# Kernel tuning notes

Hardware: AMD Instinct MI355X
Metric: run time of the kernel (lower is better)

## Reference

```python
import jax, jax.numpy as jnp
import numpy as np

N = 100000
E = 1600000

def _graphconv(x, src, dst, W, b):
    # DGL GraphConv, norm='both', in_feats > out_feats path: transform then aggregate.
    ones = jnp.ones((E,), dtype=x.dtype)
    out_deg = jax.ops.segment_sum(ones, src, num_segments=N)
    in_deg = jax.ops.segment_sum(ones, dst, num_segments=N)
    out_norm = jax.lax.rsqrt(jnp.clip(out_deg, 1.0))  # D_out^{-1/2}
    in_norm = jax.lax.rsqrt(jnp.clip(in_deg, 1.0))    # D_in^{-1/2}
    h = (x * out_norm[:, None]) @ W                    # [N, out_feats]
    msg = h[src]                                       # gather over edges [E, out_feats]
    agg = jax.ops.segment_sum(msg, dst, num_segments=N)
    return agg * in_norm[:, None] + b


def setup_inputs() -> dict:
    key = jax.random.key(0)
    k1, k2, k3, k4, k5 = jax.random.split(key, 5)
    features = jax.random.normal(k1, (N, 256), dtype=jnp.float32)
    src = jax.random.randint(k2, (E,), 0, N, dtype=jnp.int32)
    dst = jax.random.randint(k3, (E,), 0, N, dtype=jnp.int32)
    # Xavier-uniform like DGL's GraphConv reset_parameters
    lim1 = float(np.sqrt(6.0 / (256 + 64)))
    lim2 = float(np.sqrt(6.0 / (64 + 40)))
    W1 = jax.random.uniform(k4, (256, 64), jnp.float32, -lim1, lim1)
    W2 = jax.random.uniform(k5, (64, 40), jnp.float32, -lim2, lim2)
    b1 = jnp.zeros((64,), jnp.float32)
    b2 = jnp.zeros((40,), jnp.float32)
    return {"features": features, "src": src, "dst": dst,
            "W1": W1, "b1": b1, "W2": W2, "b2": b2}


def reference(features, src, dst, W1, b1, W2, b2):
    x = _graphconv(features, src, dst, W1, b1)
    x = _graphconv(x, src, dst, W2, b2)
    return x
```

## Files before the change

kernel.cpp:

```cpp
#include <hip/hip_runtime.h>

#define N_NODES 100000
#define N_EDGES 1600000
#define NBUCK 391
#define HBLK 128
#define CAP 8192


__global__ __launch_bounds__(256) void coarse_hist_kernel(
    const int* __restrict__ src, const int* __restrict__ dst,
    int* __restrict__ gHD, int* __restrict__ gHS) {
    __shared__ int hd[NBUCK], hs[NBUCK];
    for (int i = threadIdx.x; i < NBUCK; i += 256) { hd[i] = 0; hs[i] = 0; }
    __syncthreads();
    for (int e = blockIdx.x * 256 + threadIdx.x; e < N_EDGES; e += HBLK * 256) {
        atomicAdd(&hd[dst[e] >> 8], 1);
        atomicAdd(&hs[src[e] >> 8], 1);
    }
    __syncthreads();
    for (int i = threadIdx.x; i < NBUCK; i += 256) {
        if (hd[i]) atomicAdd(&gHD[i], hd[i]);
        if (hs[i]) atomicAdd(&gHS[i], hs[i]);
    }
}


__global__ void coarse_scan_kernel(const int* __restrict__ gHD, const int* __restrict__ gHS,
                                   int* __restrict__ dBase, int* __restrict__ sBase) {
    __shared__ int sd[512], se[512];
    int t = threadIdx.x;
    int vd = (t < NBUCK) ? gHD[t] : 0;
    int vs = (t < NBUCK) ? gHS[t] : 0;
    sd[t] = vd; se[t] = vs;
    __syncthreads();
    for (int s = 1; s < 512; s <<= 1) {
        int ud = (t >= s) ? sd[t - s] : 0;
        int us = (t >= s) ? se[t - s] : 0;
        __syncthreads();
        sd[t] += ud; se[t] += us;
        __syncthreads();
    }
    if (t < NBUCK) { dBase[t] = sd[t] - vd; sBase[t] = se[t] - vs; }
    if (t == 0) { dBase[NBUCK] = N_EDGES; sBase[NBUCK] = N_EDGES; }
}


__global__ __launch_bounds__(256) void scatter_both_kernel(
    const int* __restrict__ src, const int* __restrict__ dst,
    const int* __restrict__ dBase, const int* __restrict__ sBase,
    int* __restrict__ dRes, int* __restrict__ sRes,
    int* __restrict__ bsrc, unsigned char* __restrict__ bdlo,
    unsigned char* __restrict__ bslo) {
    __shared__ int hd[NBUCK], hs[NBUCK], curD[NBUCK], curS[NBUCK];
    for (int i = threadIdx.x; i < NBUCK; i += 256) { hd[i] = 0; hs[i] = 0; }
    __syncthreads();
    for (int e = blockIdx.x * 256 + threadIdx.x; e < N_EDGES; e += HBLK * 256) {
        atomicAdd(&hd[dst[e] >> 8], 1);
        atomicAdd(&hs[src[e] >> 8], 1);
    }
    __syncthreads();
    for (int i = threadIdx.x; i < NBUCK; i += 256) {
        int cd = hd[i];
        curD[i] = dBase[i] + (cd ? atomicAdd(&dRes[i], cd) : 0);
        int cs = hs[i];
        curS[i] = sBase[i] + (cs ? atomicAdd(&sRes[i], cs) : 0);
    }
    __syncthreads();
    for (int e = blockIdx.x * 256 + threadIdx.x; e < N_EDGES; e += HBLK * 256) {
        int s = src[e];
        int d = dst[e];
        int pd = atomicAdd(&curD[d >> 8], 1);
        bsrc[pd] = s;
        bdlo[pd] = (unsigned char)(d & 255);
        int ps = atomicAdd(&curS[s >> 8], 1);
        bslo[ps] = (unsigned char)(s & 255);
    }
}


__global__ __launch_bounds__(256) void fine_src_kernel(
    const int* __restrict__ sBase, const unsigned char* __restrict__ bslo,
    float* __restrict__ onorm) {
    __shared__ int hist[256];
    int t = threadIdx.x, b = blockIdx.x;
    int lo = sBase[b], hi = sBase[b + 1];
    hist[t] = 0;
    __syncthreads();
    for (int p = lo + t; p < hi; p += 256) atomicAdd(&hist[bslo[p]], 1);
    __syncthreads();
    int node = b * 256 + t;
    if (node < N_NODES) onorm[node] = 1.0f / sqrtf((float)max(hist[t], 1));
}


__global__ __launch_bounds__(256) void gemm1_kernel(
    const float* __restrict__ x, const float* __restrict__ W,
    const float* __restrict__ onorm, float* __restrict__ h, int n) {
    __shared__ float As[16][128];
    __shared__ float Ws[16][68];
    const int tid = threadIdx.x;
    const int tx = tid & 15;
    const int rg = tid >> 4;
    const int rowBase = blockIdx.x * 128;

    const int lr0 = tid >> 2;
    const int lkq = (tid & 3) * 4;
    const int wk = tid >> 4;
    const int wc = (tid & 15) * 4;

    const int row0 = rowBase + lr0;
    const int row1 = rowBase + 64 + lr0;
    const float sc0 = (row0 < n) ? onorm[row0] : 0.f;
    const float sc1 = (row1 < n) ? onorm[row1] : 0.f;

    float acc[8][4] = {};

    for (int k0 = 0; k0 < 256; k0 += 16) {
        *(float4*)&Ws[wk][wc] = *(const float4*)(W + (size_t)(k0 + wk) * 64 + wc);
        float4 v0 = make_float4(0.f, 0.f, 0.f, 0.f);
        float4 v1 = make_float4(0.f, 0.f, 0.f, 0.f);
        if (row0 < n) v0 = *(const float4*)(x + (size_t)row0 * 256 + k0 + lkq);
        if (row1 < n) v1 = *(const float4*)(x + (size_t)row1 * 256 + k0 + lkq);
        As[lkq + 0][lr0] = v0.x * sc0;
        As[lkq + 1][lr0] = v0.y * sc0;
        As[lkq + 2][lr0] = v0.z * sc0;
        As[lkq + 3][lr0] = v0.w * sc0;
        As[lkq + 0][64 + lr0] = v1.x * sc1;
        As[lkq + 1][64 + lr0] = v1.y * sc1;
        As[lkq + 2][64 + lr0] = v1.z * sc1;
        As[lkq + 3][64 + lr0] = v1.w * sc1;
        __syncthreads();
#pragma unroll
        for (int k = 0; k < 16; ++k) {
            float4 b = *(const float4*)&Ws[k][tx * 4];
            float4 a0 = *(const float4*)&As[k][rg * 8];
            float4 a1 = *(const float4*)&As[k][rg * 8 + 4];
            float av[8] = {a0.x, a0.y, a0.z, a0.w, a1.x, a1.y, a1.z, a1.w};
            float bv[4] = {b.x, b.y, b.z, b.w};
#pragma unroll
            for (int i = 0; i < 8; ++i)
#pragma unroll
                for (int j = 0; j < 4; ++j) acc[i][j] += av[i] * bv[j];
        }
        __syncthreads();
    }
#pragma unroll
    for (int i = 0; i < 8; ++i) {
        int row = rowBase + rg * 8 + i;
        if (row < n) {
            *(float4*)(h + (size_t)row * 64 + tx * 4) =
                make_float4(acc[i][0], acc[i][1], acc[i][2], acc[i][3]);
        }
    }
}


__global__ __launch_bounds__(1024) void agg64_fused_kernel(
    const int* __restrict__ dBase, const int* __restrict__ bsrc,
    const unsigned char* __restrict__ bdlo, const float* __restrict__ h,
    float* __restrict__ agg, float* __restrict__ inorm) {
    __shared__ int lsrc[CAP];
    __shared__ int hist[256], scn[256], cur[256];
    const int tid = threadIdx.x;
    const int b = blockIdx.x;
    const int lo = dBase[b];
    const int hi = min(dBase[b + 1], lo + CAP);
    if (tid < 256) hist[tid] = 0;
    __syncthreads();
    for (int p = lo + tid; p < hi; p += 1024) atomicAdd(&hist[bdlo[p]], 1);
    __syncthreads();
    int v = (tid < 256) ? hist[tid] : 0;
    if (tid < 256) scn[tid] = v;
    __syncthreads();
    for (int s = 1; s < 256; s <<= 1) {
        int u = 0;
        if (tid < 256 && tid >= s) u = scn[tid - s];
        __syncthreads();
        if (tid < 256 && tid >= s) scn[tid] += u;
        __syncthreads();
    }
    if (tid < 256) {
        int excl = scn[tid] - v;
        scn[tid] = excl;
        cur[tid] = excl;
        int node = b * 256 + tid;
        if (node < N_NODES) inorm[node] = 1.0f / sqrtf((float)max(v, 1));
    }
    __syncthreads();
    for (int p = lo + tid; p < hi; p += 1024) {
        int pos = atomicAdd(&cur[bdlo[p]], 1);
        lsrc[pos] = bsrc[p];
    }
    __syncthreads();

    const int w = tid >> 6, lane = tid & 63, q = lane >> 4, f = lane & 15;
    for (int nn = w; nn < 256; nn += 16) {
        int node = b * 256 + nn;
        if (node >= N_NODES) break;
        int beg = scn[nn];
        int end = beg + hist[nn];
        float4 a0 = {0.f, 0.f, 0.f, 0.f}, a1 = {0.f, 0.f, 0.f, 0.f};
        int j = beg;
        for (; j + 8 <= end; j += 8) {
            int s0 = lsrc[j + q], s1 = lsrc[j + 4 + q];
            float4 v0 = *((const float4*)(h + (size_t)s0 * 64) + f);
            float4 v1 = *((const float4*)(h + (size_t)s1 * 64) + f);
            a0.x += v0.x; a0.y += v0.y; a0.z += v0.z; a0.w += v0.w;
            a1.x += v1.x; a1.y += v1.y; a1.z += v1.z; a1.w += v1.w;
        }
        for (; j + 4 <= end; j += 4) {
            int s0 = lsrc[j + q];
            float4 v0 = *((const float4*)(h + (size_t)s0 * 64) + f);
            a0.x += v0.x; a0.y += v0.y; a0.z += v0.z; a0.w += v0.w;
        }
        if (j + q < end) {
            int s0 = lsrc[j + q];
            float4 v0 = *((const float4*)(h + (size_t)s0 * 64) + f);
            a0.x += v0.x; a0.y += v0.y; a0.z += v0.z; a0.w += v0.w;
        }
        a0.x += a1.x; a0.y += a1.y; a0.z += a1.z; a0.w += a1.w;
        a0.x += __shfl_xor(a0.x, 16); a0.y += __shfl_xor(a0.y, 16);
        a0.z += __shfl_xor(a0.z, 16); a0.w += __shfl_xor(a0.w, 16);
        a0.x += __shfl_xor(a0.x, 32); a0.y += __shfl_xor(a0.y, 32);
        a0.z += __shfl_xor(a0.z, 32); a0.w += __shfl_xor(a0.w, 32);
        if (q == 0) ((float4*)(agg + (size_t)node * 64))[f] = a0;
    }
}


__global__ __launch_bounds__(256) void gemm2_kernel(
    const float* __restrict__ agg, const float* __restrict__ W2,
    const float* __restrict__ b1, const float* __restrict__ inorm,
    const float* __restrict__ onorm, float* __restrict__ h2, int n) {
    const int lane = threadIdx.x & 63;
    const int wid = __builtin_amdgcn_readfirstlane(threadIdx.x >> 6);
    const int rowBase = (blockIdx.x * 4 + wid) * 8;
    const int cl = lane < 40 ? lane : 39;

    float w[64];
#pragma unroll
    for (int k = 0; k < 64; ++k) w[k] = W2[k * 40 + cl];

    float c2 = 0.f;
#pragma unroll
    for (int k = 0; k < 64; ++k) c2 += b1[k] * w[k];

#pragma unroll
    for (int r = 0; r < 8; ++r) {
        int row = rowBase + r;
        if (row < n) {
            const float* ar = agg + (size_t)row * 64;
            float acc = 0.f;
#pragma unroll
            for (int k = 0; k < 64; ++k) acc += ar[k] * w[k];
            float so = onorm[row];
            float s12 = inorm[row] * so;
            if (lane < 40) h2[(size_t)row * 40 + lane] = acc * s12 + so * c2;
        }
    }
}


__global__ __launch_bounds__(1024) void agg40_fused_kernel(
    const int* __restrict__ dBase, const int* __restrict__ bsrc,
    const unsigned char* __restrict__ bdlo, const float* __restrict__ h2,
    const float* __restrict__ b2, float* __restrict__ out) {
    __shared__ int lsrc[CAP];
    __shared__ int hist[256], scn[256], cur[256];
    const int tid = threadIdx.x;
    const int b = blockIdx.x;
    const int lo = dBase[b];
    const int hi = min(dBase[b + 1], lo + CAP);
    if (tid < 256) hist[tid] = 0;
    __syncthreads();
    for (int p = lo + tid; p < hi; p += 1024) atomicAdd(&hist[bdlo[p]], 1);
    __syncthreads();
    int v = (tid < 256) ? hist[tid] : 0;
    if (tid < 256) scn[tid] = v;
    __syncthreads();
    for (int s = 1; s < 256; s <<= 1) {
        int u = 0;
        if (tid < 256 && tid >= s) u = scn[tid - s];
        __syncthreads();
        if (tid < 256 && tid >= s) scn[tid] += u;
        __syncthreads();
    }
    if (tid < 256) {
        int excl = scn[tid] - v;
        scn[tid] = excl;
        cur[tid] = excl;
    }
    __syncthreads();
    for (int p = lo + tid; p < hi; p += 1024) {
        int pos = atomicAdd(&cur[bdlo[p]], 1);
        lsrc[pos] = bsrc[p];
    }
    __syncthreads();

    const int w = tid >> 6, lane = tid & 63, q = lane >> 4, f = lane & 15;
    const bool act = (f < 10);
    float4 vb = make_float4(0.f, 0.f, 0.f, 0.f);
    if (act) vb = ((const float4*)b2)[f];
    for (int nn = w; nn < 256; nn += 16) {
        int node = b * 256 + nn;
        if (node >= N_NODES) break;
        int beg = scn[nn];
        int end = beg + hist[nn];
        float4 a0 = {0.f, 0.f, 0.f, 0.f}, a1 = {0.f, 0.f, 0.f, 0.f};
        int j = beg;
        for (; j + 8 <= end; j += 8) {
            int s0 = lsrc[j + q], s1 = lsrc[j + 4 + q];
            if (act) {
                float4 v0 = *((const float4*)(h2 + (size_t)s0 * 40) + f);
                float4 v1 = *((const float4*)(h2 + (size_t)s1 * 40) + f);
                a0.x += v0.x; a0.y += v0.y; a0.z += v0.z; a0.w += v0.w;
                a1.x += v1.x; a1.y += v1.y; a1.z += v1.z; a1.w += v1.w;
            }
        }
        for (; j + 4 <= end; j += 4) {
            int s0 = lsrc[j + q];
            if (act) {
                float4 v0 = *((const float4*)(h2 + (size_t)s0 * 40) + f);
                a0.x += v0.x; a0.y += v0.y; a0.z += v0.z; a0.w += v0.w;
            }
        }
        if (j + q < end && act) {
            int s0 = lsrc[j + q];
            float4 v0 = *((const float4*)(h2 + (size_t)s0 * 40) + f);
            a0.x += v0.x; a0.y += v0.y; a0.z += v0.z; a0.w += v0.w;
        }
        a0.x += a1.x; a0.y += a1.y; a0.z += a1.z; a0.w += a1.w;
        a0.x += __shfl_xor(a0.x, 16); a0.y += __shfl_xor(a0.y, 16);
        a0.z += __shfl_xor(a0.z, 16); a0.w += __shfl_xor(a0.w, 16);
        a0.x += __shfl_xor(a0.x, 32); a0.y += __shfl_xor(a0.y, 32);
        a0.z += __shfl_xor(a0.z, 32); a0.w += __shfl_xor(a0.w, 32);
        if (q == 0 && act) {
            float s = 1.0f / sqrtf((float)max(hist[nn], 1));
            float4 r;
            r.x = a0.x * s + vb.x; r.y = a0.y * s + vb.y;
            r.z = a0.z * s + vb.z; r.w = a0.w * s + vb.w;
            ((float4*)(out + (size_t)node * 40))[f] = r;
        }
    }
}

extern "C" void kernel_launch(void* const* d_in, const int* in_sizes, int n_in,
                              void* d_out, int out_size, void* d_ws, size_t ws_size,
                              hipStream_t stream) {
    const float* x  = (const float*)d_in[0];
    const int* src  = (const int*)d_in[1];
    const int* dst  = (const int*)d_in[2];
    const float* W1 = (const float*)d_in[3];
    const float* b1 = (const float*)d_in[4];
    const float* W2 = (const float*)d_in[5];
    const float* b2 = (const float*)d_in[6];
    float* out = (float*)d_out;

    char* wsb = (char*)d_ws;
    size_t off = 0;
    auto alloc = [&](size_t bytes) { char* p = wsb + off; off += (bytes + 255) & ~size_t(255); return p; };

    int*   zeroed = (int*)  alloc(4 * NBUCK * 4);
    int*   gHD    = zeroed;
    int*   gHS    = zeroed + NBUCK;
    int*   dRes   = zeroed + 2 * NBUCK;
    int*   sRes   = zeroed + 3 * NBUCK;
    int*   dBase  = (int*)  alloc((NBUCK + 1) * 4);
    int*   sBase  = (int*)  alloc((NBUCK + 1) * 4);
    float* onorm  = (float*)alloc(N_NODES * 4);
    float* inorm  = (float*)alloc(N_NODES * 4);
    int*   bsrc   = (int*)  alloc((size_t)N_EDGES * 4);
    unsigned char* bdlo = (unsigned char*)alloc(N_EDGES);
    unsigned char* bslo = (unsigned char*)alloc(N_EDGES);
    float* h1     = (float*)alloc((size_t)N_NODES * 64 * 4);
    float* agg1   = (float*)alloc((size_t)N_NODES * 64 * 4);
    float* h2 = h1;

    hipMemsetAsync(zeroed, 0, 4 * NBUCK * 4, stream);

    coarse_hist_kernel<<<HBLK, 256, 0, stream>>>(src, dst, gHD, gHS);
    coarse_scan_kernel<<<1, 512, 0, stream>>>(gHD, gHS, dBase, sBase);
    scatter_both_kernel<<<HBLK, 256, 0, stream>>>(src, dst, dBase, sBase, dRes, sRes,
                                                  bsrc, bdlo, bslo);
    fine_src_kernel<<<NBUCK, 256, 0, stream>>>(sBase, bslo, onorm);

    gemm1_kernel<<<(N_NODES + 127) / 128, 256, 0, stream>>>(x, W1, onorm, h1, N_NODES);

    agg64_fused_kernel<<<NBUCK, 1024, 0, stream>>>(dBase, bsrc, bdlo, h1, agg1, inorm);

    gemm2_kernel<<<(N_NODES + 31) / 32, 256, 0, stream>>>(agg1, W2, b1, inorm, onorm, h2, N_NODES);

    agg40_fused_kernel<<<NBUCK, 1024, 0, stream>>>(dBase, bsrc, bdlo, h2, b2, out);
}
```

Before: 437.4 us.

## Halve bucket width, pack edge src/dst-low, and register-prefetch gemm1

Bucket width drops from 256 to 128 nodes (782 buckets), so the agg kernels use 512-thread blocks with a smaller LDS edge cap. Source id and destination low bits are packed into one int per edge, which removes the separate byte array and one read stream. gemm1 moves to 128 threads with an 8x8 register tile, prefetches the next x/W tile into registers, and applies onorm in the epilogue. The smaller CAP (4096 edges per bucket) could truncate edges in dense buckets, and the larger per-thread tile raises register pressure.

```diff
diff --git a/kernel.cpp b/kernel.cpp
--- a/kernel.cpp
+++ b/kernel.cpp
@@ -2,9 +2,11 @@
 
 #define N_NODES 100000
 #define N_EDGES 1600000
-#define NBUCK 391
-#define HBLK 128
-#define CAP 8192
+#define BSH 7
+#define NBUCK 782
+#define BMASK 127
+#define HBLK 512
+#define CAP 4096
 
 
 __global__ __launch_bounds__(256) void coarse_hist_kernel(
@@ -14,8 +16,8 @@
     for (int i = threadIdx.x; i < NBUCK; i += 256) { hd[i] = 0; hs[i] = 0; }
     __syncthreads();
     for (int e = blockIdx.x * 256 + threadIdx.x; e < N_EDGES; e += HBLK * 256) {
-        atomicAdd(&hd[dst[e] >> 8], 1);
-        atomicAdd(&hs[src[e] >> 8], 1);
+        atomicAdd(&hd[dst[e] >> BSH], 1);
+        atomicAdd(&hs[src[e] >> BSH], 1);
     }
     __syncthreads();
     for (int i = threadIdx.x; i < NBUCK; i += 256) {
@@ -25,15 +27,16 @@
 }
 
 
-__global__ void coarse_scan_kernel(const int* __restrict__ gHD, const int* __restrict__ gHS,
-                                   int* __restrict__ dBase, int* __restrict__ sBase) {
-    __shared__ int sd[512], se[512];
+__global__ __launch_bounds__(1024) void coarse_scan_kernel(
+    const int* __restrict__ gHD, const int* __restrict__ gHS,
+    int* __restrict__ dBase, int* __restrict__ sBase) {
+    __shared__ int sd[1024], se[1024];
     int t = threadIdx.x;
     int vd = (t < NBUCK) ? gHD[t] : 0;
     int vs = (t < NBUCK) ? gHS[t] : 0;
     sd[t] = vd; se[t] = vs;
     __syncthreads();
-    for (int s = 1; s < 512; s <<= 1) {
+    for (int s = 1; s < 1024; s <<= 1) {
         int ud = (t >= s) ? sd[t - s] : 0;
         int us = (t >= s) ? se[t - s] : 0;
         __syncthreads();
@@ -49,14 +52,13 @@
     const int* __restrict__ src, const int* __restrict__ dst,
     const int* __restrict__ dBase, const int* __restrict__ sBase,
     int* __restrict__ dRes, int* __restrict__ sRes,
-    int* __restrict__ bsrc, unsigned char* __restrict__ bdlo,
-    unsigned char* __restrict__ bslo) {
+    int* __restrict__ bpack, unsigned char* __restrict__ bslo) {
     __shared__ int hd[NBUCK], hs[NBUCK], curD[NBUCK], curS[NBUCK];
     for (int i = threadIdx.x; i < NBUCK; i += 256) { hd[i] = 0; hs[i] = 0; }
     __syncthreads();
     for (int e = blockIdx.x * 256 + threadIdx.x; e < N_EDGES; e += HBLK * 256) {
-        atomicAdd(&hd[dst[e] >> 8], 1);
-        atomicAdd(&hs[src[e] >> 8], 1);
+        atomicAdd(&hd[dst[e] >> BSH], 1);
+        atomicAdd(&hs[src[e] >> BSH], 1);
     }
     __syncthreads();
     for (int i = threadIdx.x; i < NBUCK; i += 256) {
@@ -69,11 +71,10 @@
     for (int e = blockIdx.x * 256 + threadIdx.x; e < N_EDGES; e += HBLK * 256) {
         int s = src[e];
         int d = dst[e];
-        int pd = atomicAdd(&curD[d >> 8], 1);
-        bsrc[pd] = s;
-        bdlo[pd] = (unsigned char)(d & 255);
-        int ps = atomicAdd(&curS[s >> 8], 1);
-        bslo[ps] = (unsigned char)(s & 255);
+        int pd = atomicAdd(&curD[d >> BSH], 1);
+        bpack[pd] = (s << BSH) | (d & BMASK);
+        int ps = atomicAdd(&curS[s >> BSH], 1);
+        bslo[ps] = (unsigned char)(s & BMASK);
     }
 }
 
@@ -81,121 +82,142 @@
 __global__ __launch_bounds__(256) void fine_src_kernel(
     const int* __restrict__ sBase, const unsigned char* __restrict__ bslo,
     float* __restrict__ onorm) {
-    __shared__ int hist[256];
+    __shared__ int hist[128];
     int t = threadIdx.x, b = blockIdx.x;
     int lo = sBase[b], hi = sBase[b + 1];
-    hist[t] = 0;
+    if (t < 128) hist[t] = 0;
     __syncthreads();
     for (int p = lo + t; p < hi; p += 256) atomicAdd(&hist[bslo[p]], 1);
     __syncthreads();
-    int node = b * 256 + t;
-    if (node < N_NODES) onorm[node] = 1.0f / sqrtf((float)max(hist[t], 1));
-}
-
-
-__global__ __launch_bounds__(256) void gemm1_kernel(
+    int node = b * 128 + t;
+    if (t < 128 && node < N_NODES) onorm[node] = 1.0f / sqrtf((float)max(hist[t], 1));
+}
+
+
+__global__ __launch_bounds__(128) void gemm1_kernel(
     const float* __restrict__ x, const float* __restrict__ W,
     const float* __restrict__ onorm, float* __restrict__ h, int n) {
     __shared__ float As[16][128];
     __shared__ float Ws[16][68];
     const int tid = threadIdx.x;
-    const int tx = tid & 15;
-    const int rg = tid >> 4;
+    const int tx = tid & 7;
+    const int ry = tid >> 3;
     const int rowBase = blockIdx.x * 128;
 
-    const int lr0 = tid >> 2;
-    const int lkq = (tid & 3) * 4;
-    const int wk = tid >> 4;
-    const int wc = (tid & 15) * 4;
-
-    const int row0 = rowBase + lr0;
-    const int row1 = rowBase + 64 + lr0;
-    const float sc0 = (row0 < n) ? onorm[row0] : 0.f;
-    const float sc1 = (row1 < n) ? onorm[row1] : 0.f;
-
-    float acc[8][4] = {};
-
+    const int lr = tid >> 2;
+    const int kq = (tid & 3) * 4;
+    const int wk = tid >> 3;
+    const int wc = (tid & 7) * 8;
+
+    float4 va[4], vw0, vw1;
+
+    auto load_regs = [&](int k0) {
+#pragma unroll
+        for (int p = 0; p < 4; ++p) {
+            int row = rowBase + p * 32 + lr;
+            va[p] = (row < n) ? *(const float4*)(x + (size_t)row * 256 + k0 + kq)
+                              : make_float4(0.f, 0.f, 0.f, 0.f);
+        }
+        vw0 = *(const float4*)(W + (size_t)wk * 64 + wc);
+        vw1 = *(const float4*)(W + (size_t)wk * 64 + wc + 4);
+    };
+    auto load_regs_w = [&](int k0) {
+#pragma unroll
+        for (int p = 0; p < 4; ++p) {
+            int row = rowBase + p * 32 + lr;
+            va[p] = (row < n) ? *(const float4*)(x + (size_t)row * 256 + k0 + kq)
+                              : make_float4(0.f, 0.f, 0.f, 0.f);
+        }
+        vw0 = *(const float4*)(W + (size_t)(k0 + wk) * 64 + wc);
+        vw1 = *(const float4*)(W + (size_t)(k0 + wk) * 64 + wc + 4);
+    };
+
+    float acc[8][8] = {};
+
+    load_regs(0);
     for (int k0 = 0; k0 < 256; k0 += 16) {
-        *(float4*)&Ws[wk][wc] = *(const float4*)(W + (size_t)(k0 + wk) * 64 + wc);
-        float4 v0 = make_float4(0.f, 0.f, 0.f, 0.f);
-        float4 v1 = make_float4(0.f, 0.f, 0.f, 0.f);
-        if (row0 < n) v0 = *(const float4*)(x + (size_t)row0 * 256 + k0 + lkq);
-        if (row1 < n) v1 = *(const float4*)(x + (size_t)row1 * 256 + k0 + lkq);
-        As[lkq + 0][lr0] = v0.x * sc0;
-        As[lkq + 1][lr0] = v0.y * sc0;
-        As[lkq + 2][lr0] = v0.z * sc0;
-        As[lkq + 3][lr0] = v0.w * sc0;
-        As[lkq + 0][64 + lr0] = v1.x * sc1;
-        As[lkq + 1][64 + lr0] = v1.y * sc1;
-        As[lkq + 2][64 + lr0] = v1.z * sc1;
-        As[lkq + 3][64 + lr0] = v1.w * sc1;
-        __syncthreads();
+#pragma unroll
+        for (int p = 0; p < 4; ++p) {
+            int r = p * 32 + lr;
+            As[kq + 0][r] = va[p].x;
+            As[kq + 1][r] = va[p].y;
+            As[kq + 2][r] = va[p].z;
+            As[kq + 3][r] = va[p].w;
+        }
+        *(float4*)&Ws[wk][wc] = vw0;
+        *(float4*)&Ws[wk][wc + 4] = vw1;
+        __syncthreads();
+        if (k0 + 16 < 256) load_regs_w(k0 + 16);
 #pragma unroll
         for (int k = 0; k < 16; ++k) {
-            float4 b = *(const float4*)&Ws[k][tx * 4];
-            float4 a0 = *(const float4*)&As[k][rg * 8];
-            float4 a1 = *(const float4*)&As[k][rg * 8 + 4];
+            float4 b0 = *(const float4*)&Ws[k][tx * 8];
+            float4 b1 = *(const float4*)&Ws[k][tx * 8 + 4];
+            float4 a0 = *(const float4*)&As[k][ry * 8];
+            float4 a1 = *(const float4*)&As[k][ry * 8 + 4];
             float av[8] = {a0.x, a0.y, a0.z, a0.w, a1.x, a1.y, a1.z, a1.w};
-            float bv[4] = {b.x, b.y, b.z, b.w};
+            float bv[8] = {b0.x, b0.y, b0.z, b0.w, b1.x, b1.y, b1.z, b1.w};
 #pragma unroll
             for (int i = 0; i < 8; ++i)
 #pragma unroll
-                for (int j = 0; j < 4; ++j) acc[i][j] += av[i] * bv[j];
+                for (int j = 0; j < 8; ++j) acc[i][j] += av[i] * bv[j];
         }
         __syncthreads();
     }
 #pragma unroll
     for (int i = 0; i < 8; ++i) {
-        int row = rowBase + rg * 8 + i;
+        int row = rowBase + ry * 8 + i;
         if (row < n) {
-            *(float4*)(h + (size_t)row * 64 + tx * 4) =
-                make_float4(acc[i][0], acc[i][1], acc[i][2], acc[i][3]);
-        }
-    }
-}
-
-
-__global__ __launch_bounds__(1024) void agg64_fused_kernel(
-    const int* __restrict__ dBase, const int* __restrict__ bsrc,
-    const unsigned char* __restrict__ bdlo, const float* __restrict__ h,
-    float* __restrict__ agg, float* __restrict__ inorm) {
+            float s = onorm[row];
+            *(float4*)(h + (size_t)row * 64 + tx * 8) =
+                make_float4(acc[i][0] * s, acc[i][1] * s, acc[i][2] * s, acc[i][3] * s);
+            *(float4*)(h + (size_t)row * 64 + tx * 8 + 4) =
+                make_float4(acc[i][4] * s, acc[i][5] * s, acc[i][6] * s, acc[i][7] * s);
+        }
+    }
+}
+
+
+__global__ __launch_bounds__(512) void agg64_fused_kernel(
+    const int* __restrict__ dBase, const int* __restrict__ bpack,
+    const float* __restrict__ h, float* __restrict__ agg, float* __restrict__ inorm) {
     __shared__ int lsrc[CAP];
-    __shared__ int hist[256], scn[256], cur[256];
+    __shared__ int hist[128], scn[128], cur[128];
     const int tid = threadIdx.x;
     const int b = blockIdx.x;
     const int lo = dBase[b];
     const int hi = min(dBase[b + 1], lo + CAP);
-    if (tid < 256) hist[tid] = 0;
-    __syncthreads();
-    for (int p = lo + tid; p < hi; p += 1024) atomicAdd(&hist[bdlo[p]], 1);
-    __syncthreads();
-    int v = (tid < 256) ? hist[tid] : 0;
-    if (tid < 256) scn[tid] = v;
-    __syncthreads();
-    for (int s = 1; s < 256; s <<= 1) {
+    if (tid < 128) hist[tid] = 0;
+    __syncthreads();
+    for (int p = lo + tid; p < hi; p += 512) atomicAdd(&hist[bpack[p] & BMASK], 1);
+    __syncthreads();
+    int v = (tid < 128) ? hist[tid] : 0;
+    if (tid < 128) scn[tid] = v;
+    __syncthreads();
+    for (int s = 1; s < 128; s <<= 1) {
         int u = 0;
-        if (tid < 256 && tid >= s) u = scn[tid - s];
-        __syncthreads();
-        if (tid < 256 && tid >= s) scn[tid] += u;
-        __syncthreads();
-    }
-    if (tid < 256) {
+        if (tid < 128 && tid >= s) u = scn[tid - s];
+        __syncthreads();
+        if (tid < 128 && tid >= s) scn[tid] += u;
+        __syncthreads();
+    }
+    if (tid < 128) {
         int excl = scn[tid] - v;
         scn[tid] = excl;
         cur[tid] = excl;
-        int node = b * 256 + tid;
+        int node = b * 128 + tid;
         if (node < N_NODES) inorm[node] = 1.0f / sqrtf((float)max(v, 1));
     }
     __syncthreads();
-    for (int p = lo + tid; p < hi; p += 1024) {
-        int pos = atomicAdd(&cur[bdlo[p]], 1);
-        lsrc[pos] = bsrc[p];
+    for (int p = lo + tid; p < hi; p += 512) {
+        int pk = bpack[p];
+        int pos = atomicAdd(&cur[pk & BMASK], 1);
+        lsrc[pos] = pk >> BSH;
     }
     __syncthreads();
 
     const int w = tid >> 6, lane = tid & 63, q = lane >> 4, f = lane & 15;
-    for (int nn = w; nn < 256; nn += 16) {
-        int node = b * 256 + nn;
+    for (int nn = w; nn < 128; nn += 8) {
+        int node = b * 128 + nn;
         if (node >= N_NODES) break;
         int beg = scn[nn];
         int end = beg + hist[nn];
@@ -261,39 +283,40 @@
 }
 
 
-__global__ __launch_bounds__(1024) void agg40_fused_kernel(
-    const int* __restrict__ dBase, const int* __restrict__ bsrc,
-    const unsigned char* __restrict__ bdlo, const float* __restrict__ h2,
-    const float* __restrict__ b2, float* __restrict__ out) {
+__global__ __launch_bounds__(512) void agg40_fused_kernel(
+    const int* __restrict__ dBase, const int* __restrict__ bpack,
+    const float* __restrict__ h2, const float* __restrict__ b2,
+    float* __restrict__ out) {
     __shared__ int lsrc[CAP];
-    __shared__ int hist[256], scn[256], cur[256];
+    __shared__ int hist[128], scn[128], cur[128];
     const int tid = threadIdx.x;
     const int b = blockIdx.x;
     const int lo = dBase[b];
     const int hi = min(dBase[b + 1], lo + CAP);
-    if (tid < 256) hist[tid] = 0;
-    __syncthreads();
-    for (int p = lo + tid; p < hi; p += 1024) atomicAdd(&hist[bdlo[p]], 1);
-    __syncthreads();
-    int v = (tid < 256) ? hist[tid] : 0;
-    if (tid < 256) scn[tid] = v;
-    __syncthreads();
-    for (int s = 1; s < 256; s <<= 1) {
+    if (tid < 128) hist[tid] = 0;
+    __syncthreads();
+    for (int p = lo + tid; p < hi; p += 512) atomicAdd(&hist[bpack[p] & BMASK], 1);
+    __syncthreads();
+    int v = (tid < 128) ? hist[tid] : 0;
+    if (tid < 128) scn[tid] = v;
+    __syncthreads();
+    for (int s = 1; s < 128; s <<= 1) {
         int u = 0;
-        if (tid < 256 && tid >= s) u = scn[tid - s];
-        __syncthreads();
-        if (tid < 256 && tid >= s) scn[tid] += u;
-        __syncthreads();
-    }
-    if (tid < 256) {
+        if (tid < 128 && tid >= s) u = scn[tid - s];
+        __syncthreads();
+        if (tid < 128 && tid >= s) scn[tid] += u;
+        __syncthreads();
+    }
+    if (tid < 128) {
         int excl = scn[tid] - v;
         scn[tid] = excl;
         cur[tid] = excl;
     }
     __syncthreads();
-    for (int p = lo + tid; p < hi; p += 1024) {
-        int pos = atomicAdd(&cur[bdlo[p]], 1);
-        lsrc[pos] = bsrc[p];
+    for (int p = lo + tid; p < hi; p += 512) {
+        int pk = bpack[p];
+        int pos = atomicAdd(&cur[pk & BMASK], 1);
+        lsrc[pos] = pk >> BSH;
     }
     __syncthreads();
 
@@ -301,8 +324,8 @@
     const bool act = (f < 10);
     float4 vb = make_float4(0.f, 0.f, 0.f, 0.f);
     if (act) vb = ((const float4*)b2)[f];
-    for (int nn = w; nn < 256; nn += 16) {
-        int node = b * 256 + nn;
+    for (int nn = w; nn < 128; nn += 8) {
+        int node = b * 128 + nn;
         if (node >= N_NODES) break;
         int beg = scn[nn];
         int end = beg + hist[nn];
@@ -369,8 +392,7 @@
     int*   sBase  = (int*)  alloc((NBUCK + 1) * 4);
     float* onorm  = (float*)alloc(N_NODES * 4);
     float* inorm  = (float*)alloc(N_NODES * 4);
-    int*   bsrc   = (int*)  alloc((size_t)N_EDGES * 4);
-    unsigned char* bdlo = (unsigned char*)alloc(N_EDGES);
+    int*   bpack  = (int*)  alloc((size_t)N_EDGES * 4);
     unsigned char* bslo = (unsigned char*)alloc(N_EDGES);
     float* h1     = (float*)alloc((size_t)N_NODES * 64 * 4);
     float* agg1   = (float*)alloc((size_t)N_NODES * 64 * 4);
@@ -379,16 +401,16 @@
     hipMemsetAsync(zeroed, 0, 4 * NBUCK * 4, stream);
 
     coarse_hist_kernel<<<HBLK, 256, 0, stream>>>(src, dst, gHD, gHS);
-    coarse_scan_kernel<<<1, 512, 0, stream>>>(gHD, gHS, dBase, sBase);
+    coarse_scan_kernel<<<1, 1024, 0, stream>>>(gHD, gHS, dBase, sBase);
     scatter_both_kernel<<<HBLK, 256, 0, stream>>>(src, dst, dBase, sBase, dRes, sRes,
-                                                  bsrc, bdlo, bslo);
+                                                  bpack, bslo);
     fine_src_kernel<<<NBUCK, 256, 0, stream>>>(sBase, bslo, onorm);
 
-    gemm1_kernel<<<(N_NODES + 127) / 128, 256, 0, stream>>>(x, W1, onorm, h1, N_NODES);
-
-    agg64_fused_kernel<<<NBUCK, 1024, 0, stream>>>(dBase, bsrc, bdlo, h1, agg1, inorm);
+    gemm1_kernel<<<(N_NODES + 127) / 128, 128, 0, stream>>>(x, W1, onorm, h1, N_NODES);
+
+    agg64_fused_kernel<<<NBUCK, 512, 0, stream>>>(dBase, bpack, h1, agg1, inorm);
 
     gemm2_kernel<<<(N_NODES + 31) / 32, 256, 0, stream>>>(agg1, W2, b1, inorm, onorm, h2, N_NODES);
 
-    agg40_fused_kernel<<<NBUCK, 1024, 0, stream>>>(dBase, bsrc, bdlo, h2, b2, out);
-}
+    agg40_fused_kernel<<<NBUCK, 512, 0, stream>>>(dBase, bpack, h2, b2, out);
+}
```

Measured after the change: 432.8 us. Within noise of the previous version (-1.0%).
